# Optimization experiments

Measured on AMD Instinct MI355X. Metric: run time of the kernel, lower is better.

Reference implementation:

```python
import jax, jax.numpy as jnp
import numpy as np

B, T, D, H = 2, 2048, 1024, 16
HD = D // H


def setup_inputs() -> dict:
    key = jax.random.key(0)
    ks = jax.random.split(key, 5)
    s = 1.0 / np.sqrt(D)
    return {
        "z": jax.random.normal(ks[0], (B, T, D), jnp.float32),
        "w_q": jax.random.normal(ks[1], (D, D), jnp.float32) * s,
        "w_k": jax.random.normal(ks[2], (D, D), jnp.float32) * s,
        "w_v": jax.random.normal(ks[3], (D, D), jnp.float32) * s,
        "w_o": jax.random.normal(ks[4], (D, D), jnp.float32) * s,
    }


def reference(z, w_q, w_k, w_v, w_o):
    # projections: nn.Linear(x) = x @ W.T; weights here stored as [D, D] applied as x @ w
    q = jnp.einsum('btd,de->bte', z, w_q).reshape(B, T, H, HD).transpose(0, 2, 1, 3)  # [B,H,T,hd]
    k = jnp.einsum('btd,de->bte', z, w_k).reshape(B, T, H, HD).transpose(0, 2, 1, 3)
    v = jnp.einsum('btd,de,', z, w_v).reshape(B, T, H, HD).transpose(0, 2, 1, 3) if False else jnp.einsum('btd,de->bte', z, w_v).reshape(B, T, H, HD).transpose(0, 2, 1, 3)
    scale = 1.0 / jnp.sqrt(jnp.float32(HD))
    scores = jnp.einsum('bhqd,bhkd->bhqk', q, k) * scale  # [B,H,T,T]
    causal = jnp.triu(jnp.ones((T, T), bool), k=1)  # True above diagonal -> masked
    scores = jnp.where(causal[None, None], -jnp.inf, scores)
    attn = jax.nn.softmax(scores, axis=-1)
    ctx = jnp.einsum('bhqk,bhkd->bhqd', attn, v)  # [B,H,T,hd]
    ctx = ctx.transpose(0, 2, 1, 3).reshape(B, T, D)
    return jnp.einsum('btd,de->bte', ctx, w_o)
```

## Files before the change

kernel.cpp:

```cpp
#include <hip/hip_runtime.h>
#include <hip/hip_bf16.h>

typedef __hip_bfloat16 bf16;
typedef __attribute__((ext_vector_type(8))) short bf16x8;
typedef __attribute__((ext_vector_type(4))) float f32x4;

#define MFMA16(a, b, c) __builtin_amdgcn_mfma_f32_16x16x32_bf16(a, b, c, 0, 0, 0)

constexpr int Bc = 2, Tc = 2048, Dc = 1024, Hc = 16, HDc = 64;
constexpr int BTc = Bc * Tc;

struct alignas(16) BV8 { bf16 v[8]; };

__global__ __launch_bounds__(256)
void cast_f32_to_bf16(const float* __restrict__ in, bf16* __restrict__ out, int n) {
  int i = (blockIdx.x * 256 + threadIdx.x) * 8;
  if (i >= n) return;
  float4 a = *(const float4*)(in + i);
  float4 b = *(const float4*)(in + i + 4);
  BV8 r;
  r.v[0] = __float2bfloat16(a.x); r.v[1] = __float2bfloat16(a.y);
  r.v[2] = __float2bfloat16(a.z); r.v[3] = __float2bfloat16(a.w);
  r.v[4] = __float2bfloat16(b.x); r.v[5] = __float2bfloat16(b.y);
  r.v[6] = __float2bfloat16(b.z); r.v[7] = __float2bfloat16(b.w);
  *(BV8*)(out + i) = r;
}

__global__ __launch_bounds__(256)
void wT_kernel(const float* __restrict__ w0, const float* __restrict__ w1,
               const float* __restrict__ w2, const float* __restrict__ w3,
               bf16* __restrict__ o0, bf16* __restrict__ o1,
               bf16* __restrict__ o2, bf16* __restrict__ o3) {
  const int which = blockIdx.z;
  const float* src = which == 0 ? w0 : which == 1 ? w1 : which == 2 ? w2 : w3;
  bf16* dst = which == 0 ? o0 : which == 1 ? o1 : which == 2 ? o2 : o3;
  __shared__ float tile[32][33];
  const int tx = threadIdx.x, ty = threadIdx.y;
  const int e0 = blockIdx.x * 32, d0 = blockIdx.y * 32;
#pragma unroll
  for (int rr = 0; rr < 4; ++rr) {
    int r = ty + rr * 8;
    tile[r][tx] = src[(size_t)(d0 + r) * Dc + e0 + tx];
  }
  __syncthreads();
#pragma unroll
  for (int rr = 0; rr < 4; ++rr) {
    int r = ty + rr * 8;
    dst[(size_t)(e0 + r) * Dc + d0 + tx] = __float2bfloat16(tile[tx][r]);
  }
}

__device__ inline void store_c(float* p, float v) { *p = v; }
__device__ inline void store_c(bf16* p, float v) { *p = __float2bfloat16(v); }

template <typename CT>
__global__ __launch_bounds__(256)
void gemm_bt_kernel(const bf16* __restrict__ A, const bf16* __restrict__ Bt,
                    CT* __restrict__ C, int M, int N, int K) {
  __shared__ bf16 As[128 * 32];
  __shared__ bf16 Bs[128 * 32];
  const int t = threadIdx.x;
  const int lane = t & 63, w = t >> 6;
  const int wr = w >> 1, wc = w & 1;
  const int m0 = blockIdx.y * 128, n0 = blockIdx.x * 128;
  const int l15 = lane & 15, l4 = lane >> 4;
  const int srow = lane >> 2;
  const int scol = (lane & 3) * 8;

  f32x4 acc[4][4] = {};

  for (int k0 = 0; k0 < K; k0 += 32) {
#pragma unroll
    for (int j = 0; j < 2; ++j) {
      const int ch = j * 4 + w;
      const int row = ch * 16 + srow;
      __builtin_amdgcn_global_load_lds(
          (const __attribute__((address_space(1))) void*)(A + (size_t)(m0 + row) * K + k0 + scol),
          (__attribute__((address_space(3))) void*)(As + ch * 512), 16, 0, 0);
      __builtin_amdgcn_global_load_lds(
          (const __attribute__((address_space(1))) void*)(Bt + (size_t)(n0 + row) * K + k0 + scol),
          (__attribute__((address_space(3))) void*)(Bs + ch * 512), 16, 0, 0);
    }
    __syncthreads();

    bf16x8 af[4], bg[4];
#pragma unroll
    for (int m = 0; m < 4; ++m)
      af[m] = *(const bf16x8*)(As + (wr * 64 + m * 16 + l15) * 32 + l4 * 8);
#pragma unroll
    for (int n = 0; n < 4; ++n)
      bg[n] = *(const bf16x8*)(Bs + (wc * 64 + n * 16 + l15) * 32 + l4 * 8);
#pragma unroll
    for (int m = 0; m < 4; ++m)
#pragma unroll
      for (int n = 0; n < 4; ++n)
        acc[m][n] = MFMA16(af[m], bg[n], acc[m][n]);
    __syncthreads();
  }

#pragma unroll
  for (int m = 0; m < 4; ++m) {
    const int row = m0 + wr * 64 + m * 16 + l4 * 4;
#pragma unroll
    for (int n = 0; n < 4; ++n) {
      const int col = n0 + wc * 64 + n * 16 + l15;
#pragma unroll
      for (int r = 0; r < 4; ++r)
        store_c(&C[(size_t)(row + r) * N + col], acc[m][n][r]);
    }
  }
}

__global__ __launch_bounds__(256)
void attn_kernel(const bf16* __restrict__ Q, const bf16* __restrict__ Kg, int ldqk,
                 const bf16* __restrict__ Vt, bf16* __restrict__ O) {
  const int t = threadIdx.x;
  const int lane = t & 63, w = t >> 6;
  const int l15 = lane & 15, l4 = lane >> 4;
  const int bh = blockIdx.y, b = bh >> 4, h = bh & 15;
  const int lo = blockIdx.x;
  const int hi = 31 - lo;
  const int qlo = lo * 64 + w * 16;
  const int qhi = hi * 64 + w * 16;
  const int nch = hi + 1;

  __shared__ bf16 Ks[2][64 * 64];
  __shared__ bf16 Vs[2][64 * 64];
  __shared__ bf16 Ph[4][16][72];
  __shared__ bf16 Pl[4][16][72];

  const int srow_in = lane >> 3;
  const int scb = lane & 7;

  const bf16* qph = Q + (size_t)(b * Tc + qhi + l15) * ldqk + h * HDc + l4 * 8;
  const bf16x8 ah0 = *(const bf16x8*)(qph);
  const bf16x8 ah1 = *(const bf16x8*)(qph + 32);
  const bf16* qpl = Q + (size_t)(b * Tc + qlo + l15) * ldqk + h * HDc + l4 * 8;
  const bf16x8 al0 = *(const bf16x8*)(qpl);
  const bf16x8 al1 = *(const bf16x8*)(qpl + 32);

  f32x4 ch[4] = {}, cl[4] = {};
  float shr[4] = {}, slr[4] = {};

  auto stage = [&](int buf, int c) {
    const int kv0 = c * 64;
#pragma unroll
    for (int i = 0; i < 4; ++i) {
      const int u = w * 4 + i;
      const int ul = u & 7;
      const int row = ul * 8 + srow_in;
      const int cbs = scb ^ (row & 7);
      if (u < 8) {
        const bf16* src = Kg + (size_t)(b * Tc + kv0 + row) * ldqk + h * HDc + cbs * 8;
        __builtin_amdgcn_global_load_lds(
            (const __attribute__((address_space(1))) void*)src,
            (__attribute__((address_space(3))) void*)(Ks[buf] + ul * 512), 16, 0, 0);
      } else {
        const bf16* src = Vt + (size_t)(h * HDc + row) * BTc + b * Tc + kv0 + cbs * 8;
        __builtin_amdgcn_global_load_lds(
            (const __attribute__((address_space(1))) void*)src,
            (__attribute__((address_space(3))) void*)(Vs[buf] + ul * 512), 16, 0, 0);
      }
    }
  };

  auto qk = [&](const bf16* Kbuf, const bf16x8& a0, const bf16x8& a1, f32x4* s) {
#pragma unroll
    for (int n = 0; n < 4; ++n) {
      const int row = n * 16 + l15;
      const bf16* kr = Kbuf + row * 64;
      bf16x8 bk0 = *(const bf16x8*)(kr + ((l4 ^ (row & 7)) << 3));
      bf16x8 bk1 = *(const bf16x8*)(kr + (((4 + l4) ^ (row & 7)) << 3));
      f32x4 zz = {};
      zz = MFMA16(a0, bk0, zz);
      s[n] = MFMA16(a1, bk1, zz);
    }
  };

  auto expP = [&](f32x4* s, bf16 (*Pw)[72], float* srun, int kv0, int qb, bool mask) {
#pragma unroll
    for (int n = 0; n < 4; ++n)
#pragma unroll
      for (int r = 0; r < 4; ++r) {
        float e = __expf(s[n][r] * 0.125f);
        if (mask) {
          const int kv = kv0 + n * 16 + l15;
          const int qr = qb + l4 * 4 + r;
          e = (kv <= qr) ? e : 0.0f;
        }
        srun[r] += e;
        Pw[l4 * 4 + r][n * 16 + l15] = __float2bfloat16(e);
      }
  };

  auto pv = [&](const bf16* Vbuf, bf16 (*Pw)[72], f32x4* ctx) {
    const bf16x8 pa0 = *(const bf16x8*)(&Pw[l15][l4 * 8]);
    const bf16x8 pa1 = *(const bf16x8*)(&Pw[l15][32 + l4 * 8]);
#pragma unroll
    for (int dn = 0; dn < 4; ++dn) {
      const int row = dn * 16 + l15;
      const bf16* vr = Vbuf + row * 64;
      bf16x8 bv0 = *(const bf16x8*)(vr + ((l4 ^ (row & 7)) << 3));
      bf16x8 bv1 = *(const bf16x8*)(vr + (((4 + l4) ^ (row & 7)) << 3));
      ctx[dn] = MFMA16(pa0, bv0, ctx[dn]);
      ctx[dn] = MFMA16(pa1, bv1, ctx[dn]);
    }
  };

  stage(0, 0);
  __syncthreads();

  for (int c = 0; c <= lo; ++c) {
    const int buf = c & 1;
    if (c + 1 < nch) stage(buf ^ 1, c + 1);
    f32x4 sh4[4], sl4[4];
    qk(Ks[buf], ah0, ah1, sh4);
    qk(Ks[buf], al0, al1, sl4);
    expP(sh4, Ph[w], shr, 0, 0, false);
    expP(sl4, Pl[w], slr, c * 64, qlo, c == lo);
    pv(Vs[buf], Ph[w], ch);
    pv(Vs[buf], Pl[w], cl);
    __syncthreads();
  }
  for (int c = lo + 1; c <= hi; ++c) {
    const int buf = c & 1;
    if (c + 1 < nch) stage(buf ^ 1, c + 1);
    f32x4 sh4[4];
    qk(Ks[buf], ah0, ah1, sh4);
    expP(sh4, Ph[w], shr, c * 64, qhi, c == hi);
    pv(Vs[buf], Ph[w], ch);
    __syncthreads();
  }

#pragma unroll
  for (int r = 0; r < 4; ++r) {
    for (int msk = 1; msk < 16; msk <<= 1) {
      shr[r] += __shfl_xor(shr[r], msk);
      slr[r] += __shfl_xor(slr[r], msk);
    }
  }
#pragma unroll
  for (int dn = 0; dn < 4; ++dn)
#pragma unroll
    for (int r = 0; r < 4; ++r) {
      O[(size_t)(b * Tc + qhi + l4 * 4 + r) * Dc + h * HDc + dn * 16 + l15] =
          __float2bfloat16(ch[dn][r] / shr[r]);
      O[(size_t)(b * Tc + qlo + l4 * 4 + r) * Dc + h * HDc + dn * 16 + l15] =
          __float2bfloat16(cl[dn][r] / slr[r]);
    }
}

extern "C" void kernel_launch(void* const* d_in, const int* in_sizes, int n_in,
                              void* d_out, int out_size, void* d_ws, size_t ws_size,
                              hipStream_t stream) {
  const float* z  = (const float*)d_in[0];
  const float* wq = (const float*)d_in[1];
  const float* wk = (const float*)d_in[2];
  const float* wv = (const float*)d_in[3];
  const float* wo = (const float*)d_in[4];
  float* out = (float*)d_out;

  char* ws = (char*)d_ws;
  const size_t MB = 1ull << 20;
  bf16* zb  = (bf16*)(ws + 0 * MB);
  bf16* wqT = (bf16*)(ws + 8 * MB);
  bf16* wkT = (bf16*)(ws + 10 * MB);
  bf16* wvT = (bf16*)(ws + 12 * MB);
  bf16* woT = (bf16*)(ws + 14 * MB);
  bf16* QK  = (bf16*)(ws + 16 * MB);
  bf16* Vtb = (bf16*)(ws + 32 * MB);
  bf16* Ctx = (bf16*)(ws + 40 * MB);

  cast_f32_to_bf16<<<dim3(2048), dim3(256), 0, stream>>>(z, zb, Bc * Tc * Dc);
  wT_kernel<<<dim3(32, 32, 4), dim3(32, 8), 0, stream>>>(wq, wk, wv, wo, wqT, wkT, wvT, woT);

  gemm_bt_kernel<bf16><<<dim3(16, 32), dim3(256), 0, stream>>>(zb, wqT, QK, 4096, 2048, 1024);
  gemm_bt_kernel<bf16><<<dim3(32, 8), dim3(256), 0, stream>>>(wvT, zb, Vtb, 1024, 4096, 1024);

  attn_kernel<<<dim3(16, 32), dim3(256), 0, stream>>>(QK, QK + 1024, 2048, Vtb, Ctx);

  gemm_bt_kernel<float><<<dim3(8, 32), dim3(256), 0, stream>>>(Ctx, woT, out, 4096, 1024, 1024);
}
```

Before: 209.6 us.

## Fold softmax scale into Wq and transpose QK MFMA for packed P stores

The 1/sqrt(hd) scale is folded into the bf16 transposed Wq, removing a multiply per score. The QK MFMA operands are swapped so each lane holds four consecutive kv scores for one query row. This lets P be written with packed bf16 conversions and a single 8-byte LDS store, and reduces the row-sum to one scalar per lane with fewer shuffles. The final normalisation uses reciprocal multiplies, and rounding Wq*0.125 to bf16 is exact for a power of two.

```diff
diff --git a/kernel.cpp b/kernel.cpp
--- a/kernel.cpp
+++ b/kernel.cpp
@@ -34,6 +34,7 @@
   const int which = blockIdx.z;
   const float* src = which == 0 ? w0 : which == 1 ? w1 : which == 2 ? w2 : w3;
   bf16* dst = which == 0 ? o0 : which == 1 ? o1 : which == 2 ? o2 : o3;
+  const float scale = (which == 0) ? 0.125f : 1.0f;
   __shared__ float tile[32][33];
   const int tx = threadIdx.x, ty = threadIdx.y;
   const int e0 = blockIdx.x * 32, d0 = blockIdx.y * 32;
@@ -46,7 +47,7 @@
 #pragma unroll
   for (int rr = 0; rr < 4; ++rr) {
     int r = ty + rr * 8;
-    dst[(size_t)(e0 + r) * Dc + d0 + tx] = __float2bfloat16(tile[tx][r]);
+    dst[(size_t)(e0 + r) * Dc + d0 + tx] = __float2bfloat16(tile[tx][r] * scale);
   }
 }
 
@@ -140,7 +141,7 @@
   const bf16x8 al1 = *(const bf16x8*)(qpl + 32);
 
   f32x4 ch[4] = {}, cl[4] = {};
-  float shr[4] = {}, slr[4] = {};
+  float shr = 0.0f, slr = 0.0f;
 
   auto stage = [&](int buf, int c) {
     const int kv0 = c * 64;
@@ -172,25 +173,32 @@
       bf16x8 bk0 = *(const bf16x8*)(kr + ((l4 ^ (row & 7)) << 3));
       bf16x8 bk1 = *(const bf16x8*)(kr + (((4 + l4) ^ (row & 7)) << 3));
       f32x4 zz = {};
-      zz = MFMA16(a0, bk0, zz);
-      s[n] = MFMA16(a1, bk1, zz);
-    }
-  };
-
-  auto expP = [&](f32x4* s, bf16 (*Pw)[72], float* srun, int kv0, int qb, bool mask) {
-#pragma unroll
-    for (int n = 0; n < 4; ++n)
+      zz = MFMA16(bk0, a0, zz);
+      s[n] = MFMA16(bk1, a1, zz);
+    }
+  };
+
+  auto expP = [&](f32x4* s, bf16 (*Pw)[72], float& srun, int kv0, int qb, bool mask) {
+    const int q = qb + l15;
+#pragma unroll
+    for (int n = 0; n < 4; ++n) {
+      float e[4];
 #pragma unroll
       for (int r = 0; r < 4; ++r) {
-        float e = __expf(s[n][r] * 0.125f);
+        float v = __expf(s[n][r]);
         if (mask) {
-          const int kv = kv0 + n * 16 + l15;
-          const int qr = qb + l4 * 4 + r;
-          e = (kv <= qr) ? e : 0.0f;
+          const int kv = kv0 + n * 16 + l4 * 4 + r;
+          v = (kv <= q) ? v : 0.0f;
         }
-        srun[r] += e;
-        Pw[l4 * 4 + r][n * 16 + l15] = __float2bfloat16(e);
+        e[r] = v;
+        srun += v;
       }
+      unsigned u0, u1;
+      asm("v_cvt_pk_bf16_f32 %0, %1, %2" : "=v"(u0) : "v"(e[0]), "v"(e[1]));
+      asm("v_cvt_pk_bf16_f32 %0, %1, %2" : "=v"(u1) : "v"(e[2]), "v"(e[3]));
+      uint2 uu; uu.x = u0; uu.y = u1;
+      *(uint2*)((char*)(&Pw[l15][0]) + n * 32 + l4 * 8) = uu;
+    }
   };
 
   auto pv = [&](const bf16* Vbuf, bf16 (*Pw)[72], f32x4* ctx) {
@@ -232,21 +240,24 @@
     __syncthreads();
   }
 
+  shr += __shfl_xor(shr, 16);
+  shr += __shfl_xor(shr, 32);
+  slr += __shfl_xor(slr, 16);
+  slr += __shfl_xor(slr, 32);
+  float ihr[4], ilr[4];
 #pragma unroll
   for (int r = 0; r < 4; ++r) {
-    for (int msk = 1; msk < 16; msk <<= 1) {
-      shr[r] += __shfl_xor(shr[r], msk);
-      slr[r] += __shfl_xor(slr[r], msk);
-    }
+    ihr[r] = 1.0f / __shfl(shr, l4 * 4 + r);
+    ilr[r] = 1.0f / __shfl(slr, l4 * 4 + r);
   }
 #pragma unroll
   for (int dn = 0; dn < 4; ++dn)
 #pragma unroll
     for (int r = 0; r < 4; ++r) {
       O[(size_t)(b * Tc + qhi + l4 * 4 + r) * Dc + h * HDc + dn * 16 + l15] =
-          __float2bfloat16(ch[dn][r] / shr[r]);
+          __float2bfloat16(ch[dn][r] * ihr[r]);
       O[(size_t)(b * Tc + qlo + l4 * 4 + r) * Dc + h * HDc + dn * 16 + l15] =
-          __float2bfloat16(cl[dn][r] / slr[r]);
+          __float2bfloat16(cl[dn][r] * ilr[r]);
     }
 }
 
```

New measurement: 203.8 us. -2.8%, faster.
